# Optimization experiments

Hardware: AMD Instinct MI355X
Metric: run time of the kernel (lower is better)

The kernel has to match this reference:

```python
import jax, jax.numpy as jnp
import numpy as np
import math

BATCH, TBINS, SPATIAL = 16, 8, 16
WIN, SHIFT = 8, 4
DIM, HEADS = 1024, 16
HD = DIM // HEADS
N = WIN * WIN          # tokens per window = 64
NW = (SPATIAL // WIN) ** 2  # windows per image = 4
HIDDEN = 4 * DIM


def _static_buffers():
    ws = WIN
    # continuous relative coords table (signed log-spaced), [(2ws-1)^2, 2]
    c = np.arange(-(ws - 1), ws, dtype=np.float32) / (ws - 1)
    c = np.sign(c) * np.log2(1.0 + np.abs(c))
    gh, gw = np.meshgrid(c, c, indexing='ij')
    table = np.stack([gh, gw], axis=-1).reshape(-1, 2).astype(np.float32)
    # relative position index, [N, N]
    coords = np.stack(np.meshgrid(np.arange(ws), np.arange(ws), indexing='ij')).reshape(2, -1)
    rel = (coords[:, :, None] - coords[:, None, :]).transpose(1, 2, 0)
    rel[..., 0] += ws - 1
    rel[..., 1] += ws - 1
    rel[..., 0] *= 2 * ws - 1
    rp_idx = rel.sum(-1)  # [N, N] int
    # shifted-window attention mask, [NW, N, N]
    img = np.zeros((SPATIAL, SPATIAL), dtype=np.float32)
    slices = [slice(0, -ws), slice(-ws, -SHIFT), slice(-SHIFT, None)]
    cnt = 0
    for hs in slices:
        for wsl in slices:
            img[hs, wsl] = cnt
            cnt += 1
    mw = img.reshape(SPATIAL // ws, ws, SPATIAL // ws, ws).transpose(0, 2, 1, 3).reshape(-1, ws * ws)
    diff = mw[:, None, :] - mw[:, :, None]  # matches unsqueeze(1) - unsqueeze(2)
    attn_mask = np.where(diff != 0, np.float32(-100.0), np.float32(0.0))
    return jnp.asarray(table), jnp.asarray(rp_idx), jnp.asarray(attn_mask)

CPB_TABLE, RP_IDX, ATTN_MASK = _static_buffers()


def _window_partition(x):  # [B, H, W, C] -> [B*nW, ws, ws, C]
    b, h, w, c = x.shape
    x = x.reshape(b, h // WIN, WIN, w // WIN, WIN, c).transpose(0, 1, 3, 2, 4, 5)
    return x.reshape(-1, WIN, WIN, c)


def _window_reverse(win, h, w):  # [B*nW, ws, ws, C] -> [B, H, W, C]
    b = win.shape[0] // ((h // WIN) * (w // WIN))
    x = win.reshape(b, h // WIN, w // WIN, WIN, WIN, -1).transpose(0, 1, 3, 2, 4, 5)
    return x.reshape(b, h, w, -1)


def _layernorm(x, g, b):
    m = jnp.mean(x, -1, keepdims=True)
    v = jnp.mean((x - m) ** 2, -1, keepdims=True)
    return (x - m) * jax.lax.rsqrt(v + 1e-5) * g + b


def _l2norm(x):
    return x / jnp.maximum(jnp.linalg.norm(x, axis=-1, keepdims=True), 1e-12)


def setup_inputs() -> dict:
    key = jax.random.key(0)
    ks = jax.random.split(key, 16)
    s = 0.02
    inp = {
        'x': jax.random.normal(ks[0], (BATCH, TBINS * SPATIAL * SPATIAL, DIM), jnp.float32),
        'qkv_w': jax.random.normal(ks[1], (3 * DIM, DIM), jnp.float32) * s,
        'q_bias': jnp.zeros((DIM,), jnp.float32),
        'v_bias': jnp.zeros((DIM,), jnp.float32),
        'logit_scale': jnp.full((HEADS, 1, 1), math.log(10.0), jnp.float32),
        'cpb_w1': jax.random.normal(ks[2], (512, 2), jnp.float32) * s,
        'cpb_b1': jnp.zeros((512,), jnp.float32),
        'cpb_w2': jax.random.normal(ks[3], (HEADS, 512), jnp.float32) * s,
        'proj_w': jax.random.normal(ks[4], (DIM, DIM), jnp.float32) * s,
        'proj_b': jnp.zeros((DIM,), jnp.float32),
        'norm1_w': jnp.ones((DIM,), jnp.float32),
        'norm1_b': jnp.zeros((DIM,), jnp.float32),
        'fc1_w': jax.random.normal(ks[5], (HIDDEN, DIM), jnp.float32) * s,
        'fc1_b': jnp.zeros((HIDDEN,), jnp.float32),
        'fc2_w': jax.random.normal(ks[6], (DIM, HIDDEN), jnp.float32) * s,
        'fc2_b': jnp.zeros((DIM,), jnp.float32),
        'norm2_w': jnp.ones((DIM,), jnp.float32),
        'norm2_b': jnp.zeros((DIM,), jnp.float32),
    }
    return inp


def reference(x, qkv_w, q_bias, v_bias, logit_scale, cpb_w1, cpb_b1, cpb_w2,
              proj_w, proj_b, norm1_w, norm1_b, fc1_w, fc1_b, fc2_w, fc2_b,
              norm2_w, norm2_b):
    B, L, C = x.shape
    xs = x.reshape(B * TBINS, SPATIAL, SPATIAL, C)
    shortcut = xs
    # cyclic shift
    shifted = jnp.roll(xs, shift=(-SHIFT, -SHIFT), axis=(1, 2))
    xw = _window_partition(shifted).reshape(-1, N, C)  # [Bw, N, C]
    Bw = xw.shape[0]

    # qkv with q/v bias only (no k bias)
    qkv_bias = jnp.concatenate([q_bias, jnp.zeros_like(v_bias), v_bias])
    qkv = xw @ qkv_w.T + qkv_bias
    qkv = qkv.reshape(Bw, N, 3, HEADS, HD).transpose(2, 0, 3, 1, 4)
    q, k, v = qkv[0], qkv[1], qkv[2]  # [Bw, h, N, hd]

    # cosine attention with clamped learnable logit scale
    attn = jnp.einsum('bhnd,bhmd->bhnm', _l2norm(q), _l2norm(k))
    scale = jnp.exp(jnp.minimum(logit_scale, math.log(100.0)))  # [h,1,1]
    attn = attn * scale[None]

    # continuous relative position bias via CPB-MLP
    tbl = jax.nn.relu(CPB_TABLE @ cpb_w1.T + cpb_b1) @ cpb_w2.T  # [(2ws-1)^2, h]
    tbl = 16.0 * jax.nn.sigmoid(tbl)
    bias = tbl[RP_IDX.reshape(-1)].reshape(N, N, HEADS).transpose(2, 0, 1)  # [h,N,N]
    attn = attn + bias[None]

    # shift mask
    attn = attn.reshape(Bw // NW, NW, HEADS, N, N) + ATTN_MASK[None, :, None]
    attn = attn.reshape(Bw, HEADS, N, N)
    attn = jax.nn.softmax(attn, axis=-1)

    out = jnp.einsum('bhnm,bhmd->bhnd', attn, v)
    out = out.transpose(0, 2, 1, 3).reshape(Bw, N, C)
    out = out @ proj_w.T + proj_b

    out = _window_reverse(out.reshape(-1, WIN, WIN, C), SPATIAL, SPATIAL)
    out = jnp.roll(out, shift=(SHIFT, SHIFT), axis=(1, 2))

    # SwinV2 post-norm residuals
    xs = shortcut + _layernorm(out, norm1_w, norm1_b)
    h = jax.nn.gelu(xs @ fc1_w.T + fc1_b, approximate=False) @ fc2_w.T + fc2_b
    xs = xs + _layernorm(h, norm2_w, norm2_b)
    return xs.reshape(B, L, C)
```

## Files before the change

### kernel.cpp

```cpp
#include <hip/hip_runtime.h>
#include <hip/hip_bf16.h>
#include <math.h>

typedef __hip_bfloat16 bf16;
typedef __attribute__((ext_vector_type(8))) short short8;
typedef __attribute__((ext_vector_type(4))) short short4v;
typedef __attribute__((ext_vector_type(4))) float floatx4;
typedef __attribute__((ext_vector_type(2))) unsigned int uint2v;

#define DEV static __device__ __forceinline__

DEV float bf2f(unsigned short u) {
  union { unsigned int i; float f; } x;
  x.i = ((unsigned int)u) << 16;
  return x.f;
}
DEV unsigned short f2bf_bits(float f) {
  union { bf16 h; unsigned short u; } x;
  x.h = __float2bfloat16(f);
  return x.u;
}
DEV short8 cvt8(float4 a, float4 b) {
  short8 r;
  r[0] = (short)f2bf_bits(a.x); r[1] = (short)f2bf_bits(a.y);
  r[2] = (short)f2bf_bits(a.z); r[3] = (short)f2bf_bits(a.w);
  r[4] = (short)f2bf_bits(b.x); r[5] = (short)f2bf_bits(b.y);
  r[6] = (short)f2bf_bits(b.z); r[7] = (short)f2bf_bits(b.w);
  return r;
}

DEV float gelu_fast(float v) {
  float y = v * (1.5957691216f + 0.0713548163f * v * v);
  return __fdividef(v, 1.f + __expf(-y));
}

DEV void gload_lds16(const unsigned short* g, unsigned short* l) {
  __builtin_amdgcn_global_load_lds((const __attribute__((address_space(1))) void*)g,
                                   (__attribute__((address_space(3))) void*)l,
                                   16, 0, 0);
}

DEV int gather_win_row(int wr) {
  int bw = wr >> 6, n = wr & 63;
  int bt = bw >> 2, w2 = bw & 3;
  int wi = w2 >> 1, wj = w2 & 1;
  int r = n >> 3, c = n & 7;
  int sr = (wi * 8 + r + 4) & 15;
  int sc = (wj * 8 + c + 4) & 15;
  return bt * 256 + sr * 16 + sc;
}

enum { BIAS_SIMPLE = 0, BIAS_QKV = 1 };
enum { ACT_NONE = 0, ACT_GELU = 1 };

__global__ __launch_bounds__(256) void cvt_bf16(const float* __restrict__ in,
                                                bf16* __restrict__ out, int n) {
  int i = (blockIdx.x * 256 + threadIdx.x) * 8;
  if (i >= n) return;
  float4 a = *reinterpret_cast<const float4*>(in + i);
  float4 b = *reinterpret_cast<const float4*>(in + i + 4);
  *reinterpret_cast<short8*>((unsigned short*)out + i) = cvt8(a, b);
}

#define VMCNT(N_) asm volatile("s_waitcnt vmcnt(" #N_ ")" ::: "memory")
#define BARRIER() do { __builtin_amdgcn_s_barrier(); asm volatile("" ::: "memory"); } while (0)

#define STG(BUF, ISB, KS, KT) do { \
    char* dst_ = smem + (BUF) * 65536 + (ISB) * 32768 + (KS) * 16384; \
    gload_lds16(((ISB) ? bgp[0] : agp[0]) + (KT) * 64 + (KS) * 32, \
                (unsigned short*)(dst_ + soff0)); \
    gload_lds16(((ISB) ? bgp[1] : agp[1]) + (KT) * 64 + (KS) * 32, \
                (unsigned short*)(dst_ + soff1)); \
  } while (0)

#define CONSUME(KS, IH, DO_B) do { \
    const char* ac_ = smem + bsel * 65536 + (KS) * 16384; \
    if (DO_B) { \
      const char* bc_ = ac_ + 32768; \
      _Pragma("unroll") \
      for (int j_ = 0; j_ < 4; ++j_) \
        bfr[j_] = *reinterpret_cast<const short8*>(bc_ + bBase + j_ * 1024); \
    } \
    _Pragma("unroll") \
    for (int i_ = 0; i_ < 4; ++i_) \
      af[i_] = *reinterpret_cast<const short8*>(ac_ + aBase + ((IH) * 4 + i_) * 1024); \
    __builtin_amdgcn_s_setprio(1); \
    _Pragma("unroll") \
    for (int i_ = 0; i_ < 4; ++i_) \
      _Pragma("unroll") \
      for (int j_ = 0; j_ < 4; ++j_) \
        acc[(IH) * 4 + i_][j_] = __builtin_amdgcn_mfma_f32_16x16x32_bf16( \
            af[i_], bfr[j_], acc[(IH) * 4 + i_][j_], 0, 0, 0); \
    __builtin_amdgcn_s_setprio(0); \
  } while (0)

template <int GATHER, int BIASMODE, int ACT>
__global__ __launch_bounds__(512, 2) void gemm8p(
    const unsigned short* __restrict__ A, const unsigned short* __restrict__ B,
    const float* __restrict__ bias0, const float* __restrict__ bias1,
    bf16* __restrict__ C, int M, int N, int K)
{
  extern __shared__ __align__(16) char smem[];
  const int tid = threadIdx.x;
  const int lane = tid & 63;
  const int wave = tid >> 6;
  const int wm = wave >> 2, wn = wave & 3;

  const int gx = gridDim.x;
  const int nwg = gx * gridDim.y;
  int lin = blockIdx.y * gx + blockIdx.x;
  if ((nwg & 7) == 0) lin = (lin & 7) * (nwg >> 3) + (lin >> 3);
  const int tileM = (lin % gx) * 256;
  const int tileN = (lin / gx) * 256;

  const unsigned short* agp[2];
  const unsigned short* bgp[2];
#pragma unroll
  for (int u = 0; u < 2; ++u) {
    int s = u * 512 + tid;
    int row = s >> 2, slot = s & 3;
    int gr = tileM + row;
    int sr = GATHER ? gather_win_row(gr) : gr;
    agp[u] = A + (size_t)sr * (size_t)K + slot * 8;
    bgp[u] = B + (size_t)(tileN + row) * (size_t)K + slot * 8;
  }
  const int soff0 = tid * 16;
  const int soff1 = (512 + tid) * 16;

  const int aBase = (wm * 128 + (lane & 15)) * 64 + (lane >> 4) * 16;
  const int bBase = (wn * 64 + (lane & 15)) * 64 + (lane >> 4) * 16;

  floatx4 acc[8][4];
#pragma unroll
  for (int i = 0; i < 8; ++i)
#pragma unroll
    for (int j = 0; j < 4; ++j) acc[i][j] = (floatx4){0.f, 0.f, 0.f, 0.f};

  short8 af[4], bfr[4];
  const int NT = K >> 6;
  int bsel = 0;

  STG(0, 0, 0, 0); STG(0, 1, 0, 0); STG(0, 0, 1, 0); STG(0, 1, 1, 0);
  VMCNT(0);
  BARRIER();

  for (int t = 0; t < NT - 1; ++t) {
    const int nb = bsel ^ 1;
    const int kt1 = t + 1;
    STG(nb, 0, 0, kt1); VMCNT(6); BARRIER(); CONSUME(0, 0, 1);
    STG(nb, 1, 0, kt1); VMCNT(6); BARRIER(); CONSUME(0, 1, 0);
    STG(nb, 0, 1, kt1); VMCNT(6); BARRIER(); CONSUME(1, 0, 1);
    STG(nb, 1, 1, kt1); VMCNT(6); BARRIER(); CONSUME(1, 1, 0);
    bsel = nb;
  }
  VMCNT(4); BARRIER();
  CONSUME(0, 0, 1);
  CONSUME(0, 1, 0);
  VMCNT(0); BARRIER();
  CONSUME(1, 0, 1);
  CONSUME(1, 1, 0);

  __syncthreads();
  unsigned short* sh16 = (unsigned short*)smem;
  const int g = lane >> 4, q = lane & 15;
  float bv[4];
#pragma unroll
  for (int j = 0; j < 4; ++j) {
    const int colG = tileN + wn * 64 + j * 16 + q;
    if (BIASMODE == BIAS_QKV) {
      bv[j] = (colG < 1024) ? bias0[colG] : (colG < 2048 ? 0.f : bias1[colG - 2048]);
    } else {
      bv[j] = bias0[colG];
    }
  }
#pragma unroll
  for (int h = 0; h < 2; ++h) {
    if (wm == h) {
#pragma unroll
      for (int i = 0; i < 8; ++i)
#pragma unroll
        for (int j = 0; j < 4; ++j)
#pragma unroll
          for (int r = 0; r < 4; ++r) {
            float v = acc[i][j][r] + bv[j];
            if (ACT == ACT_GELU) v = gelu_fast(v);
            sh16[(i * 16 + g * 4 + r) * 264 + wn * 64 + j * 16 + q] = f2bf_bits(v);
          }
    }
    __syncthreads();
#pragma unroll
    for (int pass = 0; pass < 8; ++pass) {
      const int idx = pass * 512 + tid;
      const int row = idx >> 5, c16 = idx & 31;
      uint4 val = *reinterpret_cast<const uint4*>(&sh16[row * 264 + c16 * 8]);
      *reinterpret_cast<uint4*>(
          (unsigned short*)C + (size_t)(tileM + h * 128 + row) * (size_t)N +
          tileN + c16 * 8) = val;
    }
    __syncthreads();
  }
}

template <int GATHER, int BIASMODE, int ACT>
__global__ __launch_bounds__(256, 2) void gemm_bt(
    const unsigned short* __restrict__ A, const unsigned short* __restrict__ B,
    const float* __restrict__ bias0, const float* __restrict__ bias1,
    bf16* __restrict__ C, int M, int N, int K)
{
  __shared__ __align__(16) unsigned short sh[128 * 136];
  unsigned short* As = sh;
  unsigned short* Bs = sh + 8192;

  const int tid = threadIdx.x;
  const int lane = tid & 63;
  const int wave = tid >> 6;
  const int waveM = wave >> 1, waveN = wave & 1;
  const int tileM = blockIdx.x * 128, tileN = blockIdx.y * 128;

  const int row0 = tid >> 3;
  const int kOff = (tid & 7) * 8;

  const unsigned short* ag[4];
  const unsigned short* bg[4];
  unsigned short* al[4];
  unsigned short* bl[4];
#pragma unroll
  for (int t = 0; t < 4; ++t) {
    int gr = tileM + row0 + 32 * t;
    int sr = GATHER ? gather_win_row(gr) : gr;
    ag[t] = A + (size_t)sr * (size_t)K + (size_t)kOff;
    bg[t] = B + (size_t)(tileN + row0 + 32 * t) * (size_t)K + (size_t)kOff;
    al[t] = &As[(row0 + 32 * t) * 64 + kOff];
    bl[t] = &Bs[(row0 + 32 * t) * 64 + kOff];
  }

  floatx4 acc[4][4];
#pragma unroll
  for (int i = 0; i < 4; ++i)
#pragma unroll
    for (int j = 0; j < 4; ++j) acc[i][j] = (floatx4){0.f, 0.f, 0.f, 0.f};

  for (int k0 = 0; k0 < K; k0 += 64) {
#pragma unroll
    for (int t = 0; t < 4; ++t) {
      gload_lds16(ag[t] + k0, al[t]);
      gload_lds16(bg[t] + k0, bl[t]);
    }
    __syncthreads();
#pragma unroll
    for (int ks = 0; ks < 2; ++ks) {
      const int kk = ks * 32 + (lane >> 4) * 8;
      short8 afv[4], bfv[4];
#pragma unroll
      for (int i = 0; i < 4; ++i)
        afv[i] = *reinterpret_cast<const short8*>(
            &As[(waveM * 64 + i * 16 + (lane & 15)) * 64 + kk]);
#pragma unroll
      for (int j = 0; j < 4; ++j)
        bfv[j] = *reinterpret_cast<const short8*>(
            &Bs[(waveN * 64 + j * 16 + (lane & 15)) * 64 + kk]);
#pragma unroll
      for (int i = 0; i < 4; ++i)
#pragma unroll
        for (int j = 0; j < 4; ++j)
          acc[i][j] = __builtin_amdgcn_mfma_f32_16x16x32_bf16(afv[i], bfv[j], acc[i][j], 0, 0, 0);
    }
    __syncthreads();
  }

#pragma unroll
  for (int j = 0; j < 4; ++j) {
    const int colL = waveN * 64 + j * 16 + (lane & 15);
    const int colG = tileN + colL;
    float bv;
    if (BIASMODE == BIAS_QKV) {
      if (colG < 1024) bv = bias0[colG];
      else if (colG < 2048) bv = 0.f;
      else bv = bias1[colG - 2048];
    } else {
      bv = bias0[colG];
    }
#pragma unroll
    for (int i = 0; i < 4; ++i) {
      const int rL = waveM * 64 + i * 16 + ((lane >> 4) * 4);
#pragma unroll
      for (int r = 0; r < 4; ++r) {
        float v = acc[i][j][r] + bv;
        if (ACT == ACT_GELU) v = gelu_fast(v);
        sh[(rL + r) * 136 + colL] = f2bf_bits(v);
      }
    }
  }
  __syncthreads();
  {
    const int rowR = tid >> 4;
    const int colR = (tid & 15) * 8;
#pragma unroll
    for (int s = 0; s < 8; ++s) {
      const int row = s * 16 + rowR;
      uint4 val = *reinterpret_cast<const uint4*>(&sh[row * 136 + colR]);
      *reinterpret_cast<uint4*>(
          (unsigned short*)C + (size_t)(tileM + row) * (size_t)N + tileN + colR) = val;
    }
  }
}

__global__ __launch_bounds__(512) void cpb_kernel(
    const float* __restrict__ w1, const float* __restrict__ b1,
    const float* __restrict__ w2, float* __restrict__ TBL)
{
  __shared__ float hid[512];
  const int i = blockIdx.x;
  const int j = threadIdx.x;
  const float d0 = ((float)(i / 15) - 7.f) / 7.f;
  const float d1 = ((float)(i % 15) - 7.f) / 7.f;
  const float t0 = copysignf(log2f(1.f + fabsf(d0)), d0);
  const float t1 = copysignf(log2f(1.f + fabsf(d1)), d1);
  float hv = t0 * w1[j * 2] + t1 * w1[j * 2 + 1] + b1[j];
  hid[j] = fmaxf(hv, 0.f);
  __syncthreads();
  if (j < 16) {
    float s = 0.f;
    for (int jj = 0; jj < 512; ++jj) s += w2[j * 512 + jj] * hid[jj];
    TBL[j * 225 + i] = 16.f / (1.f + expf(-s));
  }
}

__global__ __launch_bounds__(256) void attn_mfma(
    const bf16* __restrict__ QKV, const float* __restrict__ TBL,
    const float* __restrict__ ls, bf16* __restrict__ ATT)
{
  __shared__ __align__(16) unsigned short Ps[4][64][72];
  __shared__ float tbs[4][226];
  __shared__ int ids[64];

  const int tid = threadIdx.x;
  const int w = tid >> 6;
  const int l = tid & 63;
  const int q = l & 15;
  const int g = l >> 4;
  const int bw = blockIdx.x >> 2;
  const int h = (blockIdx.x & 3) * 4 + w;

  const unsigned short* qkvu = (const unsigned short*)QKV;
  const size_t rbase = (size_t)(bw * 64) * 3072;

  if (tid < 64) {
    const int w2 = bw & 3, wi = w2 >> 1, wj = w2 & 1;
    const int r = tid >> 3, c = tid & 7;
    const int rr = (wi == 0) ? 0 : (r < 4 ? 1 : 2);
    const int rc = (wj == 0) ? 0 : (c < 4 ? 1 : 2);
    ids[tid] = rr * 3 + rc;
  }
#pragma unroll
  for (int i = 0; i < 4; ++i) {
    int idx = i * 64 + l;
    if (idx < 225) tbs[w][idx] = TBL[h * 225 + idx];
  }
  __syncthreads();

  short8 kf[4][2], qf[4][2];
#pragma unroll
  for (int i = 0; i < 4; ++i) {
    const unsigned short* rp = qkvu + rbase + (size_t)(16 * i + q) * 3072 + h * 64 + g * 8;
    qf[i][0] = *reinterpret_cast<const short8*>(rp);
    qf[i][1] = *reinterpret_cast<const short8*>(rp + 32);
    kf[i][0] = *reinterpret_cast<const short8*>(rp + 1024);
    kf[i][1] = *reinterpret_cast<const short8*>(rp + 1024 + 32);
  }

  float rk4[4], rq4[4];
#pragma unroll
  for (int i = 0; i < 4; ++i) {
    float sk = 0.f, sq = 0.f;
#pragma unroll
    for (int ks = 0; ks < 2; ++ks)
#pragma unroll
      for (int e = 0; e < 8; ++e) {
        float kv = bf2f((unsigned short)kf[i][ks][e]);
        float qv = bf2f((unsigned short)qf[i][ks][e]);
        sk += kv * kv; sq += qv * qv;
      }
    sk += __shfl_xor(sk, 16); sk += __shfl_xor(sk, 32);
    sq += __shfl_xor(sq, 16); sq += __shfl_xor(sq, 32);
    rk4[i] = 1.f / fmaxf(sqrtf(sk), 1e-12f);
    rq4[i] = 1.f / fmaxf(sqrtf(sq), 1e-12f);
  }
  const float scl = expf(fminf(ls[h], 4.60517019f));
  float rqs[4];
#pragma unroll
  for (int j = 0; j < 4; ++j) rqs[j] = rq4[j] * scl;

  floatx4 acc[4][4];
#pragma unroll
  for (int i = 0; i < 4; ++i)
#pragma unroll
    for (int j = 0; j < 4; ++j) acc[i][j] = (floatx4){0.f, 0.f, 0.f, 0.f};
#pragma unroll
  for (int ks = 0; ks < 2; ++ks)
#pragma unroll
    for (int i = 0; i < 4; ++i)
#pragma unroll
      for (int j = 0; j < 4; ++j)
        acc[i][j] = __builtin_amdgcn_mfma_f32_16x16x32_bf16(kf[i][ks], qf[j][ks], acc[i][j], 0, 0, 0);

  short8 vf[4][2];
  const unsigned short* vbase = qkvu + rbase + 2048 + h * 64;
#pragma unroll
  for (int jp = 0; jp < 4; ++jp)
#pragma unroll
    for (int ks = 0; ks < 2; ++ks) {
      const int m0 = ks * 32 + g * 8;
      const unsigned short* vp = vbase + 16 * jp + q;
      union { short8 v; unsigned short u[8]; } pk;
#pragma unroll
      for (int e = 0; e < 8; ++e)
        pk.u[e] = vp[(size_t)(m0 + e) * 3072];
      vf[jp][ks] = pk.v;
    }

  int idn[4], rtn[4], ctn[4];
#pragma unroll
  for (int j = 0; j < 4; ++j) {
    const int n = 16 * j + q;
    rtn[j] = n >> 3; ctn[j] = n & 7; idn[j] = ids[n];
  }
#pragma unroll
  for (int i = 0; i < 4; ++i) {
#pragma unroll
    for (int r = 0; r < 4; ++r) {
      const int m = 16 * i + 4 * g + r;
      const float rkm = __shfl(rk4[i], 4 * g + r);
      const int rm = m >> 3, cm = m & 7;
      const int idm = ids[m];
#pragma unroll
      for (int j = 0; j < 4; ++j) {
        float v = acc[i][j][r] * (rkm * rqs[j]) +
                  tbs[w][(rtn[j] - rm + 7) * 15 + (ctn[j] - cm + 7)];
        if (idm != idn[j]) v -= 100.f;
        acc[i][j][r] = v;
      }
    }
  }

  float rs4[4];
#pragma unroll
  for (int j = 0; j < 4; ++j) {
    float mx = acc[0][j][0];
#pragma unroll
    for (int i = 0; i < 4; ++i)
#pragma unroll
      for (int r = 0; r < 4; ++r) mx = fmaxf(mx, acc[i][j][r]);
    mx = fmaxf(mx, __shfl_xor(mx, 16));
    mx = fmaxf(mx, __shfl_xor(mx, 32));
    float sm = 0.f;
#pragma unroll
    for (int i = 0; i < 4; ++i)
#pragma unroll
      for (int r = 0; r < 4; ++r) {
        float e = __expf(acc[i][j][r] - mx);
        acc[i][j][r] = e; sm += e;
      }
    sm += __shfl_xor(sm, 16);
    sm += __shfl_xor(sm, 32);
    rs4[j] = 1.f / sm;
  }

#pragma unroll
  for (int j = 0; j < 4; ++j)
#pragma unroll
    for (int i = 0; i < 4; ++i) {
      uint2v pw;
      pw[0] = (unsigned int)f2bf_bits(acc[i][j][0]) |
              ((unsigned int)f2bf_bits(acc[i][j][1]) << 16);
      pw[1] = (unsigned int)f2bf_bits(acc[i][j][2]) |
              ((unsigned int)f2bf_bits(acc[i][j][3]) << 16);
      *reinterpret_cast<uint2v*>(&Ps[w][16 * j + q][16 * i + 4 * g]) = pw;
    }

  floatx4 o[4][4];
#pragma unroll
  for (int i = 0; i < 4; ++i)
#pragma unroll
    for (int j = 0; j < 4; ++j) o[i][j] = (floatx4){0.f, 0.f, 0.f, 0.f};
#pragma unroll
  for (int ks = 0; ks < 2; ++ks) {
    short8 pa[4];
#pragma unroll
    for (int i2 = 0; i2 < 4; ++i2)
      pa[i2] = *reinterpret_cast<const short8*>(&Ps[w][16 * i2 + q][ks * 32 + g * 8]);
#pragma unroll
    for (int i2 = 0; i2 < 4; ++i2)
#pragma unroll
      for (int j2 = 0; j2 < 4; ++j2)
        o[i2][j2] = __builtin_amdgcn_mfma_f32_16x16x32_bf16(pa[i2], vf[j2][ks], o[i2][j2], 0, 0, 0);
  }

  unsigned short* op = (unsigned short*)ATT + (size_t)(bw * 64) * 1024 + h * 64;
#pragma unroll
  for (int i2 = 0; i2 < 4; ++i2)
#pragma unroll
    for (int r = 0; r < 4; ++r) {
      const float rsn = __shfl(rs4[i2], 4 * g + r);
      const int row = 16 * i2 + 4 * g + r;
#pragma unroll
      for (int j2 = 0; j2 < 4; ++j2)
        op[(size_t)row * 1024 + 16 * j2 + q] = f2bf_bits(o[i2][j2][r] * rsn);
    }
}

template <bool GATHER, bool WB>
__global__ __launch_bounds__(256) void ln_residual(
    const bf16* __restrict__ src, const float* base,
    const float* __restrict__ gw, const float* __restrict__ gb,
    float* out, bf16* __restrict__ out_bf)
{
  const int tok = blockIdx.x * 4 + (threadIdx.x >> 6);
  const int lane = threadIdx.x & 63;
  int srow;
  if (GATHER) {
    const int bt = tok >> 8, rem = tok & 255, i = rem >> 4, j = rem & 15;
    const int p = (i + 12) & 15, qq = (j + 12) & 15;
    srow = (bt * 4 + (p >> 3) * 2 + (qq >> 3)) * 64 + (p & 7) * 8 + (qq & 7);
  } else {
    srow = tok;
  }
  const unsigned short* sp = (const unsigned short*)src + (size_t)srow * 1024 + lane * 16;
  short8 lv0 = *reinterpret_cast<const short8*>(sp);
  short8 lv1 = *reinterpret_cast<const short8*>(sp + 8);
  float v[16];
  float s = 0.f, sq = 0.f;
#pragma unroll
  for (int u = 0; u < 8; ++u) {
    float f = bf2f((unsigned short)lv0[u]); v[u] = f; s += f; sq += f * f;
    float g = bf2f((unsigned short)lv1[u]); v[u + 8] = g; s += g; sq += g * g;
  }
#pragma unroll
  for (int off = 32; off > 0; off >>= 1) { s += __shfl_xor(s, off); sq += __shfl_xor(sq, off); }
  const float mean = s * (1.f / 1024.f);
  const float var = sq * (1.f / 1024.f) - mean * mean;
  const float rstd = rsqrtf(var + 1e-5f);

  const float* bp = base + (size_t)tok * 1024 + lane * 16;
  float* op = out + (size_t)tok * 1024 + lane * 16;
  unsigned short* obp = WB ? ((unsigned short*)out_bf + (size_t)tok * 1024 + lane * 16) : nullptr;
  union { short8 v; unsigned short u[8]; } ob0, ob1;
#pragma unroll
  for (int q4 = 0; q4 < 4; ++q4) {
    float4 b4 = *reinterpret_cast<const float4*>(bp + q4 * 4);
    float bl[4] = {b4.x, b4.y, b4.z, b4.w};
    float4 o4;
    float* ol = (float*)&o4;
#pragma unroll
    for (int u = 0; u < 4; ++u) {
      const int c = lane * 16 + q4 * 4 + u;
      ol[u] = bl[u] + (v[q4 * 4 + u] - mean) * rstd * gw[c] + gb[c];
      if (WB) {
        if (q4 < 2) ob0.u[q4 * 4 + u] = f2bf_bits(ol[u]);
        else ob1.u[(q4 - 2) * 4 + u] = f2bf_bits(ol[u]);
      }
    }
    *reinterpret_cast<float4*>(op + q4 * 4) = o4;
  }
  if (WB) {
    *reinterpret_cast<short8*>(obp) = ob0.v;
    *reinterpret_cast<short8*>(obp + 8) = ob1.v;
  }
}

extern "C" void kernel_launch(void* const* d_in, const int* in_sizes, int n_in,
                              void* d_out, int out_size, void* d_ws, size_t ws_size,
                              hipStream_t stream) {
  (void)in_sizes; (void)n_in; (void)out_size;
  const float* x      = (const float*)d_in[0];
  const float* qkv_w  = (const float*)d_in[1];
  const float* q_bias = (const float*)d_in[2];
  const float* v_bias = (const float*)d_in[3];
  const float* lscale = (const float*)d_in[4];
  const float* cpb_w1 = (const float*)d_in[5];
  const float* cpb_b1 = (const float*)d_in[6];
  const float* cpb_w2 = (const float*)d_in[7];
  const float* proj_w = (const float*)d_in[8];
  const float* proj_b = (const float*)d_in[9];
  const float* n1w    = (const float*)d_in[10];
  const float* n1b    = (const float*)d_in[11];
  const float* fc1_w  = (const float*)d_in[12];
  const float* fc1_b  = (const float*)d_in[13];
  const float* fc2_w  = (const float*)d_in[14];
  const float* fc2_b  = (const float*)d_in[15];
  const float* n2w    = (const float*)d_in[16];
  const float* n2b    = (const float*)d_in[17];
  float* out = (float*)d_out;

  static int attr_ok = -1;
  if (attr_ok < 0) {
    hipError_t e1 = hipFuncSetAttribute(
        reinterpret_cast<const void*>(&gemm8p<1, BIAS_QKV, ACT_NONE>),
        hipFuncAttributeMaxDynamicSharedMemorySize, 131072);
    hipError_t e2 = hipFuncSetAttribute(
        reinterpret_cast<const void*>(&gemm8p<0, BIAS_SIMPLE, ACT_NONE>),
        hipFuncAttributeMaxDynamicSharedMemorySize, 131072);
    hipError_t e3 = hipFuncSetAttribute(
        reinterpret_cast<const void*>(&gemm8p<0, BIAS_SIMPLE, ACT_GELU>),
        hipFuncAttributeMaxDynamicSharedMemorySize, 131072);
    attr_ok = (e1 == hipSuccess && e2 == hipSuccess && e3 == hipSuccess) ? 1 : 0;
  }

  char* ws = (char*)d_ws;
  bf16*  QKV  = (bf16*)(ws);
  bf16*  H    = (bf16*)(ws);
  bf16*  ATT  = (bf16*)(ws + 67108864);
  bf16*  XSB  = (bf16*)(ws + 67108864);
  bf16*  F2   = (bf16*)(ws + 67108864);
  bf16*  XBF  = (bf16*)(ws + 83886080);
  bf16*  PROJ = (bf16*)(ws + 83886080);
  float* TBL  = (float*)(ws + 100663296);

  const bool persist = ws_size >= (size_t)125845504;
  bf16* WQKV, *WPROJ, *WF1, *WF2;
  if (persist) {
    WQKV  = (bf16*)(ws + 100679680);
    WPROJ = (bf16*)(ws + 106971136);
    WF1   = (bf16*)(ws + 109068288);
    WF2   = (bf16*)(ws + 117456896);
  } else {
    WQKV  = (bf16*)(ws + 67108864);
    WPROJ = (bf16*)(ws + 50331648);
    WF1   = (bf16*)(ws + 83886080);
    WF2   = (bf16*)(ws + 83886080 + 8388608);
  }

  cpb_kernel<<<225, 512, 0, stream>>>(cpb_w1, cpb_b1, cpb_w2, TBL);
  if (persist) {
    cvt_bf16<<<1536, 256, 0, stream>>>(qkv_w, WQKV, 3145728);
    cvt_bf16<<<512, 256, 0, stream>>>(proj_w, WPROJ, 1048576);
    cvt_bf16<<<2048, 256, 0, stream>>>(fc1_w, WF1, 4194304);
    cvt_bf16<<<2048, 256, 0, stream>>>(fc2_w, WF2, 4194304);
  }

  for (int ch = 0; ch < 4; ++ch) {
    const size_t tokBase = (size_t)ch * 8192;
    const float* x_c = x + tokBase * 1024;
    float* out_c = out + tokBase * 1024;

    cvt_bf16<<<4096, 256, 0, stream>>>(x_c, XBF, 8388608);
    if (!persist) {
      cvt_bf16<<<1536, 256, 0, stream>>>(qkv_w, WQKV, 3145728);
      cvt_bf16<<<512, 256, 0, stream>>>(proj_w, WPROJ, 1048576);
    }

    if (attr_ok) {
      gemm8p<1, BIAS_QKV, ACT_NONE><<<dim3(32, 12), 512, 131072, stream>>>(
          (const unsigned short*)XBF, (const unsigned short*)WQKV,
          q_bias, v_bias, QKV, 8192, 3072, 1024);
    } else {
      gemm_bt<1, BIAS_QKV, ACT_NONE><<<dim3(64, 24), 256, 0, stream>>>(
          (const unsigned short*)XBF, (const unsigned short*)WQKV,
          q_bias, v_bias, QKV, 8192, 3072, 1024);
    }
    attn_mfma<<<512, 256, 0, stream>>>(QKV, TBL, lscale, ATT);
    if (attr_ok) {
      gemm8p<0, BIAS_SIMPLE, ACT_NONE><<<dim3(32, 4), 512, 131072, stream>>>(
          (const unsigned short*)ATT, (const unsigned short*)WPROJ,
          proj_b, nullptr, PROJ, 8192, 1024, 1024);
    } else {
      gemm_bt<0, BIAS_SIMPLE, ACT_NONE><<<dim3(64, 8), 256, 0, stream>>>(
          (const unsigned short*)ATT, (const unsigned short*)WPROJ,
          proj_b, nullptr, PROJ, 8192, 1024, 1024);
    }
    ln_residual<true, true><<<2048, 256, 0, stream>>>(PROJ, x_c, n1w, n1b, out_c, XSB);
    if (!persist) {
      cvt_bf16<<<2048, 256, 0, stream>>>(fc1_w, WF1, 4194304);
      cvt_bf16<<<2048, 256, 0, stream>>>(fc2_w, WF2, 4194304);
    }
    if (attr_ok) {
      gemm8p<0, BIAS_SIMPLE, ACT_GELU><<<dim3(32, 16), 512, 131072, stream>>>(
          (const unsigned short*)XSB, (const unsigned short*)WF1,
          fc1_b, nullptr, H, 8192, 4096, 1024);
      gemm8p<0, BIAS_SIMPLE, ACT_NONE><<<dim3(32, 4), 512, 131072, stream>>>(
          (const unsigned short*)H, (const unsigned short*)WF2,
          fc2_b, nullptr, F2, 8192, 1024, 4096);
    } else {
      gemm_bt<0, BIAS_SIMPLE, ACT_GELU><<<dim3(64, 32), 256, 0, stream>>>(
          (const unsigned short*)XSB, (const unsigned short*)WF1,
          fc1_b, nullptr, H, 8192, 4096, 1024);
      gemm_bt<0, BIAS_SIMPLE, ACT_NONE><<<dim3(64, 8), 256, 0, stream>>>(
          (const unsigned short*)H, (const unsigned short*)WF2,
          fc2_b, nullptr, F2, 8192, 1024, 4096);
    }
    ln_residual<false, false><<<2048, 256, 0, stream>>>(F2, out_c, n2w, n2b, out_c, nullptr);
  }
}
```

Before: 1.725 ms.

## Rework GEMM main loop with swizzled LDS, inline-asm reads, and reordered staging

New measurement: 1.713 ms. Within noise of the previous version (-0.7%).

```diff
diff --git a/kernel.cpp b/kernel.cpp
--- a/kernel.cpp
+++ b/kernel.cpp
@@ -38,6 +38,10 @@
   __builtin_amdgcn_global_load_lds((const __attribute__((address_space(1))) void*)g,
                                    (__attribute__((address_space(3))) void*)l,
                                    16, 0, 0);
+}
+
+DEV unsigned lds_addr(const void* p) {
+  return (unsigned)(unsigned long long)(const __attribute__((address_space(3))) char*)p;
 }
 
 DEV int gather_win_row(int wr) {
@@ -63,27 +67,29 @@
 }
 
 #define VMCNT(N_) asm volatile("s_waitcnt vmcnt(" #N_ ")" ::: "memory")
-#define BARRIER() do { __builtin_amdgcn_s_barrier(); asm volatile("" ::: "memory"); } while (0)
-
-#define STG(BUF, ISB, KS, KT) do { \
-    char* dst_ = smem + (BUF) * 65536 + (ISB) * 32768 + (KS) * 16384; \
-    gload_lds16(((ISB) ? bgp[0] : agp[0]) + (KT) * 64 + (KS) * 32, \
-                (unsigned short*)(dst_ + soff0)); \
-    gload_lds16(((ISB) ? bgp[1] : agp[1]) + (KT) * 64 + (KS) * 32, \
-                (unsigned short*)(dst_ + soff1)); \
+#define WAITLGKM() do { asm volatile("s_waitcnt lgkmcnt(0)" ::: "memory"); \
+                        __builtin_amdgcn_sched_barrier(0); } while (0)
+#define BARRIER() __builtin_amdgcn_s_barrier()
+#define DSR(dst, addr, OFF) \
+  asm volatile("ds_read_b128 %0, %1 offset:" #OFF : "=v"(dst) : "v"(addr) : "memory")
+
+#define STG8(BUF, ISB, KS, KT) do { \
+    unsigned short* d_ = (unsigned short*)(smem + (BUF) * 65536 + (ISB) * 32768 + (KS) * 16384); \
+    gload_lds16(((ISB) ? bgp[0] : agp[0]) + (KT) * 64 + (KS) * 32, d_ + tid * 8); \
+    gload_lds16(((ISB) ? bgp[1] : agp[1]) + (KT) * 64 + (KS) * 32, d_ + 4096 + tid * 8); \
   } while (0)
 
-#define CONSUME(KS, IH, DO_B) do { \
-    const char* ac_ = smem + bsel * 65536 + (KS) * 16384; \
-    if (DO_B) { \
-      const char* bc_ = ac_ + 32768; \
-      _Pragma("unroll") \
-      for (int j_ = 0; j_ < 4; ++j_) \
-        bfr[j_] = *reinterpret_cast<const short8*>(bc_ + bBase + j_ * 1024); \
-    } \
-    _Pragma("unroll") \
-    for (int i_ = 0; i_ < 4; ++i_) \
-      af[i_] = *reinterpret_cast<const short8*>(ac_ + aBase + ((IH) * 4 + i_) * 1024); \
+#define RD_A8(CUR, KS, IH) do { \
+    unsigned a_ = smemBase + (CUR) * 65536 + (KS) * 16384 + aB0 + (IH) * 4096; \
+    DSR(af[0], a_, 0); DSR(af[1], a_, 1024); DSR(af[2], a_, 2048); DSR(af[3], a_, 3072); \
+  } while (0)
+
+#define RD_B8(CUR, KS) do { \
+    unsigned b_ = smemBase + (CUR) * 65536 + 32768 + (KS) * 16384 + bB0; \
+    DSR(bfr[0], b_, 0); DSR(bfr[1], b_, 1024); DSR(bfr[2], b_, 2048); DSR(bfr[3], b_, 3072); \
+  } while (0)
+
+#define MFMA16(IH) do { \
     __builtin_amdgcn_s_setprio(1); \
     _Pragma("unroll") \
     for (int i_ = 0; i_ < 4; ++i_) \
@@ -105,30 +111,32 @@
   const int lane = tid & 63;
   const int wave = tid >> 6;
   const int wm = wave >> 2, wn = wave & 3;
-
-  const int gx = gridDim.x;
-  const int nwg = gx * gridDim.y;
-  int lin = blockIdx.y * gx + blockIdx.x;
+  const int l15 = lane & 15, g = lane >> 4;
+  const int xr = (l15 >> 1) & 3;
+
+  const int gy = gridDim.y;
+  const int nwg = gridDim.x * gy;
+  int lin = blockIdx.y * gridDim.x + blockIdx.x;
   if ((nwg & 7) == 0) lin = (lin & 7) * (nwg >> 3) + (lin >> 3);
-  const int tileM = (lin % gx) * 256;
-  const int tileN = (lin / gx) * 256;
+  const int tileM = (lin / gy) * 256;
+  const int tileN = (lin % gy) * 256;
 
   const unsigned short* agp[2];
   const unsigned short* bgp[2];
 #pragma unroll
   for (int u = 0; u < 2; ++u) {
     int s = u * 512 + tid;
-    int row = s >> 2, slot = s & 3;
+    int row = s >> 2;
+    int dslot = (s & 3) ^ ((s >> 3) & 3);
     int gr = tileM + row;
     int sr = GATHER ? gather_win_row(gr) : gr;
-    agp[u] = A + (size_t)sr * (size_t)K + slot * 8;
-    bgp[u] = B + (size_t)(tileN + row) * (size_t)K + slot * 8;
-  }
-  const int soff0 = tid * 16;
-  const int soff1 = (512 + tid) * 16;
-
-  const int aBase = (wm * 128 + (lane & 15)) * 64 + (lane >> 4) * 16;
-  const int bBase = (wn * 64 + (lane & 15)) * 64 + (lane >> 4) * 16;
+    agp[u] = A + (size_t)sr * (size_t)K + dslot * 8;
+    bgp[u] = B + (size_t)(tileN + row) * (size_t)K + dslot * 8;
+  }
+
+  const unsigned smemBase = lds_addr(smem);
+  const unsigned aB0 = (unsigned)((wm * 128 + l15) * 64 + ((g ^ xr) * 16));
+  const unsigned bB0 = (unsigned)((wn * 64 + l15) * 64 + ((g ^ xr) * 16));
 
   floatx4 acc[8][4];
 #pragma unroll
@@ -138,31 +146,43 @@
 
   short8 af[4], bfr[4];
   const int NT = K >> 6;
-  int bsel = 0;
-
-  STG(0, 0, 0, 0); STG(0, 1, 0, 0); STG(0, 0, 1, 0); STG(0, 1, 1, 0);
+  int cur = 0;
+
+  STG8(0, 0, 0, 0); STG8(0, 1, 0, 0); STG8(0, 0, 1, 0); STG8(0, 1, 1, 0);
   VMCNT(0);
   BARRIER();
 
   for (int t = 0; t < NT - 1; ++t) {
-    const int nb = bsel ^ 1;
-    const int kt1 = t + 1;
-    STG(nb, 0, 0, kt1); VMCNT(6); BARRIER(); CONSUME(0, 0, 1);
-    STG(nb, 1, 0, kt1); VMCNT(6); BARRIER(); CONSUME(0, 1, 0);
-    STG(nb, 0, 1, kt1); VMCNT(6); BARRIER(); CONSUME(1, 0, 1);
-    STG(nb, 1, 1, kt1); VMCNT(6); BARRIER(); CONSUME(1, 1, 0);
-    bsel = nb;
-  }
-  VMCNT(4); BARRIER();
-  CONSUME(0, 0, 1);
-  CONSUME(0, 1, 0);
-  VMCNT(0); BARRIER();
-  CONSUME(1, 0, 1);
-  CONSUME(1, 1, 0);
+    const int nb = cur ^ 1;
+    RD_B8(cur, 0); RD_A8(cur, 0, 0);
+    STG8(nb, 0, 0, t + 1);
+    BARRIER(); WAITLGKM(); MFMA16(0); BARRIER();
+    RD_A8(cur, 0, 1);
+    STG8(nb, 1, 0, t + 1);
+    VMCNT(4);
+    BARRIER(); WAITLGKM(); MFMA16(1); BARRIER();
+    RD_B8(cur, 1); RD_A8(cur, 1, 0);
+    STG8(nb, 0, 1, t + 1);
+    BARRIER(); WAITLGKM(); MFMA16(0); BARRIER();
+    RD_A8(cur, 1, 1);
+    STG8(nb, 1, 1, t + 1);
+    VMCNT(4);
+    BARRIER(); WAITLGKM(); MFMA16(1); BARRIER();
+    cur = nb;
+  }
+  RD_B8(cur, 0); RD_A8(cur, 0, 0);
+  BARRIER(); WAITLGKM(); MFMA16(0); BARRIER();
+  RD_A8(cur, 0, 1);
+  VMCNT(0);
+  BARRIER(); WAITLGKM(); MFMA16(1); BARRIER();
+  RD_B8(cur, 1); RD_A8(cur, 1, 0);
+  BARRIER(); WAITLGKM(); MFMA16(0); BARRIER();
+  RD_A8(cur, 1, 1);
+  WAITLGKM(); MFMA16(1);
 
   __syncthreads();
   unsigned short* sh16 = (unsigned short*)smem;
-  const int g = lane >> 4, q = lane & 15;
+  const int q = l15;
   float bv[4];
 #pragma unroll
   for (int j = 0; j < 4; ++j) {
```
